# Performance work log

Measured on AMD Instinct MI355X. Metric: run time of the kernel, lower is better.

The kernel has to match this reference:

```python
import jax, jax.numpy as jnp
import numpy as np

B, S, D, H = 4, 2048, 1024, 16
HD = D // H

def setup_inputs() -> dict:
    key = jax.random.key(0)
    ks = jax.random.split(key, 12)
    std = 1.0 / np.sqrt(D)
    inp = {
        'query': jax.random.normal(ks[0], (B, S, D), jnp.float32),
        'key':   jax.random.normal(ks[1], (B, S, D), jnp.float32),
        'value': jax.random.normal(ks[2], (B, S, D), jnp.float32),
        'mask':  jnp.tril(jnp.ones((S, S), jnp.int32))[None, None, :, :],  # [1,1,S,S] causal
        'Wq': jax.random.uniform(ks[3], (D, D), jnp.float32, -std, std),
        'bq': jax.random.uniform(ks[4], (D,), jnp.float32, -std, std),
        'Wk': jax.random.uniform(ks[5], (D, D), jnp.float32, -std, std),
        'bk': jax.random.uniform(ks[6], (D,), jnp.float32, -std, std),
        'Wv': jax.random.uniform(ks[7], (D, D), jnp.float32, -std, std),
        'bv': jax.random.uniform(ks[8], (D,), jnp.float32, -std, std),
        'Wo': jax.random.uniform(ks[9], (D, D), jnp.float32, -std, std),
        'bo': jax.random.uniform(ks[10], (D,), jnp.float32, -std, std),
    }
    return inp

def _split_heads(x, W, b):
    # torch Linear: x @ W.T + b ; then [B,S,H,HD] -> [B,H,S,HD]
    y = jnp.einsum('bsd,ed->bse', x, W) + b
    return y.reshape(x.shape[0], -1, H, HD).transpose(0, 2, 1, 3)

def reference(query, key, value, mask, Wq, bq, Wk, bk, Wv, bv, Wo, bo):
    q = _split_heads(query, Wq, bq)   # [B,H,S,HD]
    k = _split_heads(key,   Wk, bk)
    v = _split_heads(value, Wv, bv)
    logits = jnp.einsum('bhqd,bhkd->bhqk', q, k) / np.sqrt(HD)  # [B,H,S,S]
    logits = jnp.where(mask == 0, jnp.float32(-1e9), logits)
    attn = jax.nn.softmax(logits, axis=-1)
    out = jnp.einsum('bhqk,bhkd->bhqd', attn, v)               # [B,H,S,HD]
    out = out.transpose(0, 2, 1, 3).reshape(query.shape[0], -1, D)
    return jnp.einsum('bsd,ed->bse', out, Wo) + bo
```

## Files before the change

### kernel.cpp

```cpp
#include <hip/hip_runtime.h>
#include <hip/hip_bf16.h>


#define SLEN 2048
#define DMOD 1024

typedef __attribute__((ext_vector_type(8))) short s16x8;
typedef __attribute__((ext_vector_type(4))) float f32x4;

__device__ __forceinline__ unsigned short f2bf(float f) {
    union { __hip_bfloat16 h; unsigned short u; } cv;
    cv.h = __float2bfloat16(f);
    return cv.u;
}
__device__ __forceinline__ unsigned cvtpk(float a, float b) {
    unsigned r;
    asm("v_cvt_pk_bf16_f32 %0, %1, %2" : "=v"(r) : "v"(a), "v"(b));
    return r;
}

__device__ __forceinline__ void gload_lds16(const void* g, void* l) {
    __builtin_amdgcn_global_load_lds(
        (const __attribute__((address_space(1))) void*)g,
        (__attribute__((address_space(3))) void*)l, 16, 0, 0);
}

__global__ __launch_bounds__(256) void convert_bf16(
    const float* __restrict__ q, const float* __restrict__ k,
    const float* __restrict__ v, const float* __restrict__ wq,
    const float* __restrict__ wk, const float* __restrict__ wv,
    const float* __restrict__ wo, unsigned short* __restrict__ ws)
{
    const int bid = blockIdx.x, tid = threadIdx.x;
    const float* src;
    unsigned short* dst;
    size_t off;
    if (bid < 3072) {
        const int t = bid >> 10;
        src = (t == 0) ? q : (t == 1) ? k : v;
        dst = ws + (size_t)t * 8388608;
        off = (size_t)(bid & 1023) * 8192;
    } else {
        const int w = (bid - 3072) >> 7;
        src = (w == 0) ? wq : (w == 1) ? wk : (w == 2) ? wv : wo;
        dst = ws + 25165824 + (size_t)w * 1048576;
        off = (size_t)((bid - 3072) & 127) * 8192;
    }
#pragma unroll
    for (int i = 0; i < 8; ++i) {
        const size_t e = off + (size_t)(i * 256 + tid) * 4;
        float4 x = *reinterpret_cast<const float4*>(&src[e]);
        uint2 u;
        u.x = cvtpk(x.x, x.y);
        u.y = cvtpk(x.z, x.w);
        *reinterpret_cast<uint2*>(&dst[e]) = u;
    }
}

template<int MODE>
__global__ __launch_bounds__(256) void gemm_bf16(
    const unsigned short* __restrict__ A, const unsigned short* __restrict__ W,
    const float* __restrict__ bias, void* __restrict__ outp, float oscale)
{
    __shared__ unsigned short Asm[2][8192];
    __shared__ unsigned short Bsm[2][8192];

    const int tid  = threadIdx.x;
    const int lane = tid & 63, wid = tid >> 6;
    const int l15 = lane & 15, lhi = lane >> 4;

    const int flat = blockIdx.x;
    const int logical = (flat & 7) * 64 + (flat >> 3);
    const int m0 = (logical >> 3) * 128, n0 = (logical & 7) * 128;

    const int wr = wid >> 1, wc = wid & 1;
    const int srow = lane >> 3;
    const int sgr  = (lane & 7) ^ srow;

    int aoff[2][4], boff[2][4];
#pragma unroll
    for (int kk = 0; kk < 2; ++kk)
#pragma unroll
        for (int i = 0; i < 4; ++i) {
            const int s = ((4 * kk + lhi) ^ (l15 & 7)) * 16;
            aoff[kk][i] = (wr * 64 + i * 16 + l15) * 128 + s;
            boff[kk][i] = (wc * 64 + i * 16 + l15) * 128 + s;
        }

    const unsigned short* apt = A + (size_t)(m0 + wid * 8 + srow) * 1024 + sgr * 8;
    const unsigned short* bpt = W + (size_t)(n0 + wid * 8 + srow) * 1024 + sgr * 8;

    f32x4 acc[4][4];
#pragma unroll
    for (int i = 0; i < 4; ++i)
#pragma unroll
        for (int j = 0; j < 4; ++j) acc[i][j] = (f32x4)0.f;

    auto stage = [&](int bsel) {
        char* ad = (char*)Asm + bsel * 16384 + wid * 1024;
        char* bd = (char*)Bsm + bsel * 16384 + wid * 1024;
#pragma unroll
        for (int i = 0; i < 4; ++i) {
            gload_lds16(apt + i * 32768, ad + i * 4096);
            gload_lds16(bpt + i * 32768, bd + i * 4096);
        }
        apt += 64; bpt += 64;
    };

    stage(0);
    __syncthreads();
    int cur = 0;
#pragma unroll 1
    for (int kt = 0; kt < 16; ++kt) {
        if (kt < 15) stage(cur ^ 1);
        const char* AB = (const char*)Asm + cur * 16384;
        const char* BB = (const char*)Bsm + cur * 16384;
#pragma unroll
        for (int kk = 0; kk < 2; ++kk) {
            s16x8 af[4], bfv[4];
#pragma unroll
            for (int i = 0; i < 4; ++i) af[i]  = *reinterpret_cast<const s16x8*>(AB + aoff[kk][i]);
#pragma unroll
            for (int j = 0; j < 4; ++j) bfv[j] = *reinterpret_cast<const s16x8*>(BB + boff[kk][j]);
#pragma unroll
            for (int i = 0; i < 4; ++i)
#pragma unroll
                for (int j = 0; j < 4; ++j)
                    acc[i][j] = __builtin_amdgcn_mfma_f32_16x16x32_bf16(af[i], bfv[j], acc[i][j], 0, 0, 0);
        }
        __syncthreads();
        cur ^= 1;
    }

#pragma unroll
    for (int j = 0; j < 4; ++j) {
        const int col = n0 + wc * 64 + j * 16 + l15;
        const float bv = bias[col];
#pragma unroll
        for (int i = 0; i < 4; ++i) {
#pragma unroll
            for (int r = 0; r < 4; ++r) {
                const int row = m0 + wr * 64 + i * 16 + lhi * 4 + r;
                const float val = (acc[i][j][r] + bv) * oscale;
                if constexpr (MODE == 2) {
                    ((float*)outp)[(size_t)row * 1024 + col] = val;
                } else if constexpr (MODE == 0) {
                    ((unsigned short*)outp)[(size_t)((row >> 11) * 16 + (col >> 6)) * 131072
                                            + (size_t)(row & 2047) * 64 + (col & 63)] = f2bf(val);
                } else {
                    ((unsigned short*)outp)[(size_t)((row >> 11) * 16 + (col >> 6)) * 131072
                                            + (size_t)(col & 63) * 2048 + (row & 2047)] = f2bf(val);
                }
            }
        }
    }
}

#define EXPC 0.18033688011112043f

__global__ __launch_bounds__(256, 4) void attn_kernel(
    const unsigned short* __restrict__ Q,
    const unsigned short* __restrict__ Kc,
    const unsigned short* __restrict__ Vt,
    unsigned short* __restrict__ Ao)
{
    __shared__ char smem[40960];

    const int tid = threadIdx.x, lane = tid & 63, wid = tid >> 6;
    const int l15 = lane & 15, lhi = lane >> 4;
    const int sK = l15 & 7;
    const int sub = lane >> 3, c8s = lane & 7;
    const int thr = wid * 16 + l15;

    const int kb0 = l15 * 128 + (lhi ^ sK) * 16;
    const int kb1 = kb0 ^ 64;
    char* const pb0 = smem + 32768 + wid * 2048 + kb0;
    char* const pb1 = smem + 32768 + wid * 2048 + kb1;
    char* const PWp = smem + 32768 + wid * 2048;
    int pw[4];
#pragma unroll
    for (int nb = 0; nb < 4; ++nb)
        pw[nb] = (l15 * 16 + ((nb * 4 + lhi) ^ (2 * sK))) * 8;

    const int flat = blockIdx.x;
    const int logical = (flat & 7) * 128 + (flat >> 3);
    const int bx = logical & 15, bh = logical >> 4;
    const int qtL = bx, qtH = 31 - bx;
    const int q0L = qtL * 64, q0H = qtH * 64;

    const size_t base = (size_t)bh * SLEN * 64;
    const unsigned short* Qb = Q + base;
    const unsigned short* Kb = Kc + base;
    const unsigned short* Vb = Vt + base;
    const int b = bh >> 4, h = bh & 15;
    const int scol = (c8s ^ sub) * 8;

    const f32x4 fzero = (f32x4)0.f;
    const s16x8 onesb = (s16x8)(short)0x3F80;

    s16x8 aqL[2], aqH[2];
#pragma unroll
    for (int kk = 0; kk < 2; ++kk) {
        aqL[kk] = *reinterpret_cast<const s16x8*>(
            &Qb[(size_t)(q0L + wid * 16 + l15) * 64 + kk * 32 + 8 * lhi]);
        aqH[kk] = *reinterpret_cast<const s16x8*>(
            &Qb[(size_t)(q0H + wid * 16 + l15) * 64 + kk * 32 + 8 * lhi]);
    }

    f32x4 oL[4], oH[4];
#pragma unroll
    for (int nb = 0; nb < 4; ++nb) { oL[nb] = (f32x4)0.f; oH[nb] = (f32x4)0.f; }
    f32x4 lL = (f32x4)0.f, lH = (f32x4)0.f;

    const unsigned short* kpt = Kb + (16 * wid + sub) * 64 + scol;
    const unsigned short* vpt = Vb + (size_t)(16 * wid + sub) * SLEN + scol;

    auto stage = [&](int bsel) {
        char* kd = smem + bsel * 8192 + wid * 2048;
        char* vd = smem + 16384 + bsel * 8192 + wid * 2048;
        gload_lds16(kpt,         kd);
        gload_lds16(kpt + 512,   kd + 1024);
        gload_lds16(vpt,         vd);
        gload_lds16(vpt + 16384, vd + 1024);
        kpt += 4096; vpt += 64;
    };

    auto tile = [&](s16x8 (&aq)[2], f32x4 (&o_acc)[4], f32x4& l_acc,
                    bool domask, const char* c0, const char* c1) {
        f32x4 sc2[4];
        __builtin_amdgcn_s_setprio(1);
        {
            s16x8 ak[4];
#pragma unroll
            for (int nb = 0; nb < 4; ++nb)
                ak[nb] = *reinterpret_cast<const s16x8*>(c0 + nb * 2048);
#pragma unroll
            for (int nb = 0; nb < 4; ++nb)
                sc2[nb] = __builtin_amdgcn_mfma_f32_16x16x32_bf16(ak[nb], aq[0], fzero, 0, 0, 0);
#pragma unroll
            for (int nb = 0; nb < 4; ++nb)
                ak[nb] = *reinterpret_cast<const s16x8*>(c1 + nb * 2048);
#pragma unroll
            for (int nb = 0; nb < 4; ++nb)
                sc2[nb] = __builtin_amdgcn_mfma_f32_16x16x32_bf16(ak[nb], aq[1], sc2[nb], 0, 0, 0);
        }
        __builtin_amdgcn_s_setprio(0);

        if (domask) {
#pragma unroll
            for (int nb = 0; nb < 4; ++nb)
#pragma unroll
                for (int r = 0; r < 4; ++r)
                    if (nb * 16 + lhi * 4 + r > thr) sc2[nb][r] = -1e30f;
        }

#pragma unroll
        for (int nb = 0; nb < 4; ++nb) {
            float p0 = exp2f(sc2[nb][0]);
            float p1 = exp2f(sc2[nb][1]);
            float p2 = exp2f(sc2[nb][2]);
            float p3 = exp2f(sc2[nb][3]);
            uint2 u;
            u.x = cvtpk(p0, p1);
            u.y = cvtpk(p2, p3);
            *reinterpret_cast<uint2*>(PWp + pw[nb]) = u;
        }

        __builtin_amdgcn_s_setprio(1);
#pragma unroll
        for (int kk = 0; kk < 2; ++kk) {
            s16x8 pa = *reinterpret_cast<const s16x8*>(kk ? pb1 : pb0);
            const char* vb = (kk ? c1 : c0) + 16384;
            s16x8 bvv[4];
#pragma unroll
            for (int nb = 0; nb < 4; ++nb)
                bvv[nb] = *reinterpret_cast<const s16x8*>(vb + nb * 2048);
#pragma unroll
            for (int nb = 0; nb < 4; ++nb)
                o_acc[nb] = __builtin_amdgcn_mfma_f32_16x16x32_bf16(pa, bvv[nb], o_acc[nb], 0, 0, 0);
            l_acc = __builtin_amdgcn_mfma_f32_16x16x32_bf16(pa, onesb, l_acc, 0, 0, 0);
        }
        __builtin_amdgcn_s_setprio(0);
    };

    stage(0);
    __syncthreads();
    int cur = 0;
    const int nt = qtH + 1;

#pragma unroll 1
    for (int t = 0; t < nt; ++t) {
        if (t + 1 < nt) stage(cur ^ 1);
        const char* c0 = smem + cur * 8192 + kb0;
        const char* c1 = smem + cur * 8192 + kb1;
        if (t <= qtL) tile(aqL, oL, lL, t == qtL, c0, c1);
        tile(aqH, oH, lH, t == qtH, c0, c1);
        __syncthreads();
        cur ^= 1;
    }

    float liL[4], liH[4];
#pragma unroll
    for (int r = 0; r < 4; ++r) { liL[r] = 1.0f / lL[r]; liH[r] = 1.0f / lH[r]; }
#pragma unroll
    for (int nb = 0; nb < 4; ++nb)
#pragma unroll
        for (int r = 0; r < 4; ++r) {
            const int sL = q0L + wid * 16 + lhi * 4 + r;
            const int sH = q0H + wid * 16 + lhi * 4 + r;
            const size_t cix = h * 64 + nb * 16 + l15;
            Ao[((size_t)b * SLEN + sL) * DMOD + cix] = f2bf(oL[nb][r] * liL[r]);
            Ao[((size_t)b * SLEN + sH) * DMOD + cix] = f2bf(oH[nb][r] * liH[r]);
        }
}

extern "C" void kernel_launch(void* const* d_in, const int* in_sizes, int n_in,
                              void* d_out, int out_size, void* d_ws, size_t ws_size,
                              hipStream_t stream) {
    const float* q  = (const float*)d_in[0];
    const float* k  = (const float*)d_in[1];
    const float* v  = (const float*)d_in[2];
    const float* Wq = (const float*)d_in[4];
    const float* bq = (const float*)d_in[5];
    const float* Wk = (const float*)d_in[6];
    const float* bk = (const float*)d_in[7];
    const float* Wv = (const float*)d_in[8];
    const float* bv = (const float*)d_in[9];
    const float* Wo = (const float*)d_in[10];
    const float* bo = (const float*)d_in[11];

    unsigned short* wsp = (unsigned short*)d_ws;
    unsigned short* qc  = wsp;
    unsigned short* kc  = wsp + 8388608;
    unsigned short* vc  = wsp + 16777216;
    unsigned short* wqc = wsp + 25165824;
    unsigned short* wkc = wsp + 26214400;
    unsigned short* wvc = wsp + 27262976;
    unsigned short* woc = wsp + 28311552;
    unsigned short* qb  = wsp + 29360128;
    unsigned short* kb  = wsp + 37748736;
    unsigned short* vtb = wsp + 46137344;
    unsigned short* ao  = qc;

    dim3 gb(256);
    convert_bf16<<<dim3(3584), gb, 0, stream>>>(q, k, v, Wq, Wk, Wv, Wo, wsp);
    gemm_bf16<0><<<dim3(512), gb, 0, stream>>>(qc, wqc, bq, qb, EXPC);
    gemm_bf16<0><<<dim3(512), gb, 0, stream>>>(kc, wkc, bk, kb, 1.0f);
    gemm_bf16<1><<<dim3(512), gb, 0, stream>>>(vc, wvc, bv, vtb, 1.0f);
    attn_kernel<<<dim3(1024), gb, 0, stream>>>(qb, kb, vtb, ao);
    gemm_bf16<2><<<dim3(512), gb, 0, stream>>>(ao, woc, bo, (float*)d_out, 1.0f);
}
```

Baseline: 178.8 us.

## Fuse fp32-to-bf16 activation conversion into QKV projection GEMM loads

```diff
diff --git a/kernel.cpp b/kernel.cpp
--- a/kernel.cpp
+++ b/kernel.cpp
@@ -25,27 +25,16 @@
         (__attribute__((address_space(3))) void*)l, 16, 0, 0);
 }
 
-__global__ __launch_bounds__(256) void convert_bf16(
-    const float* __restrict__ q, const float* __restrict__ k,
-    const float* __restrict__ v, const float* __restrict__ wq,
-    const float* __restrict__ wk, const float* __restrict__ wv,
-    const float* __restrict__ wo, unsigned short* __restrict__ ws)
+__global__ __launch_bounds__(256) void convert_w(
+    const float* __restrict__ wq, const float* __restrict__ wk,
+    const float* __restrict__ wv, const float* __restrict__ wo,
+    unsigned short* __restrict__ dst)
 {
     const int bid = blockIdx.x, tid = threadIdx.x;
-    const float* src;
-    unsigned short* dst;
-    size_t off;
-    if (bid < 3072) {
-        const int t = bid >> 10;
-        src = (t == 0) ? q : (t == 1) ? k : v;
-        dst = ws + (size_t)t * 8388608;
-        off = (size_t)(bid & 1023) * 8192;
-    } else {
-        const int w = (bid - 3072) >> 7;
-        src = (w == 0) ? wq : (w == 1) ? wk : (w == 2) ? wv : wo;
-        dst = ws + 25165824 + (size_t)w * 1048576;
-        off = (size_t)((bid - 3072) & 127) * 8192;
-    }
+    const int w = bid >> 7;
+    const float* src = (w == 0) ? wq : (w == 1) ? wk : (w == 2) ? wv : wo;
+    unsigned short* d = dst + (size_t)w * 1048576;
+    const size_t off = (size_t)(bid & 127) * 8192;
 #pragma unroll
     for (int i = 0; i < 8; ++i) {
         const size_t e = off + (size_t)(i * 256 + tid) * 4;
@@ -53,14 +42,140 @@
         uint2 u;
         u.x = cvtpk(x.x, x.y);
         u.y = cvtpk(x.z, x.w);
-        *reinterpret_cast<uint2*>(&dst[e]) = u;
+        *reinterpret_cast<uint2*>(&d[e]) = u;
     }
 }
 
 template<int MODE>
-__global__ __launch_bounds__(256) void gemm_bf16(
+__global__ __launch_bounds__(256) void gemm_qkv(
+    const float* __restrict__ A, const unsigned short* __restrict__ W,
+    const float* __restrict__ bias, unsigned short* __restrict__ outp,
+    float oscale)
+{
+    __shared__ unsigned short Asm[2][8192];
+    __shared__ unsigned short Bsm[2][8192];
+
+    const int tid  = threadIdx.x;
+    const int lane = tid & 63, wid = tid >> 6;
+    const int l15 = lane & 15, lhi = lane >> 4;
+
+    const int flat = blockIdx.x;
+    const int logical = (flat & 7) * 64 + (flat >> 3);
+    const int m0 = (logical >> 3) * 128, n0 = (logical & 7) * 128;
+    const int wr = wid >> 1, wc = wid & 1;
+
+    int soff[4];
+    const float* aptc[4];
+#pragma unroll
+    for (int i = 0; i < 4; ++i) {
+        const int f = i * 256 + tid;
+        const int srow = f >> 3, sg = f & 7;
+        soff[i] = srow * 128 + ((sg ^ (srow & 7)) * 16);
+        aptc[i] = A + (size_t)(m0 + srow) * 1024 + sg * 8;
+    }
+    const int wsrow = lane >> 3;
+    const int wsgr  = (lane & 7) ^ wsrow;
+    const unsigned short* bpt = W + (size_t)(n0 + wid * 8 + wsrow) * 1024 + wsgr * 8;
+
+    int aoff[2][4], boff[2][4];
+#pragma unroll
+    for (int kk = 0; kk < 2; ++kk)
+#pragma unroll
+        for (int i = 0; i < 4; ++i) {
+            const int s = ((4 * kk + lhi) ^ (l15 & 7)) * 16;
+            aoff[kk][i] = (wr * 64 + i * 16 + l15) * 128 + s;
+            boff[kk][i] = (wc * 64 + i * 16 + l15) * 128 + s;
+        }
+
+    f32x4 acc[4][4];
+#pragma unroll
+    for (int i = 0; i < 4; ++i)
+#pragma unroll
+        for (int j = 0; j < 4; ++j) acc[i][j] = (f32x4)0.f;
+
+    float4 aw[8];
+
+    auto loadA = [&](int k0) {
+#pragma unroll
+        for (int i = 0; i < 4; ++i) {
+            aw[2 * i]     = *reinterpret_cast<const float4*>(aptc[i] + k0);
+            aw[2 * i + 1] = *reinterpret_cast<const float4*>(aptc[i] + k0 + 4);
+        }
+    };
+    auto writeA = [&](int bsel) {
+#pragma unroll
+        for (int i = 0; i < 4; ++i) {
+            uint4 u;
+            u.x = cvtpk(aw[2 * i].x,     aw[2 * i].y);
+            u.y = cvtpk(aw[2 * i].z,     aw[2 * i].w);
+            u.z = cvtpk(aw[2 * i + 1].x, aw[2 * i + 1].y);
+            u.w = cvtpk(aw[2 * i + 1].z, aw[2 * i + 1].w);
+            *reinterpret_cast<uint4*>((char*)&Asm[bsel][0] + soff[i]) = u;
+        }
+    };
+    auto stageW = [&](int bsel) {
+        char* bd = (char*)Bsm + bsel * 16384 + wid * 1024;
+#pragma unroll
+        for (int i = 0; i < 4; ++i)
+            gload_lds16(bpt + i * 32768, bd + i * 4096);
+        bpt += 64;
+    };
+
+    loadA(0);
+    stageW(0);
+    writeA(0);
+    __syncthreads();
+
+#pragma unroll 1
+    for (int kt = 0; kt < 16; ++kt) {
+        if (kt < 15) {
+            loadA((kt + 1) * 64);
+            stageW((kt + 1) & 1);
+        }
+        const char* AB = (const char*)&Asm[kt & 1][0];
+        const char* BB = (const char*)&Bsm[kt & 1][0];
+#pragma unroll
+        for (int kk = 0; kk < 2; ++kk) {
+            s16x8 af[4], bfv[4];
+#pragma unroll
+            for (int i = 0; i < 4; ++i) af[i]  = *reinterpret_cast<const s16x8*>(AB + aoff[kk][i]);
+#pragma unroll
+            for (int j = 0; j < 4; ++j) bfv[j] = *reinterpret_cast<const s16x8*>(BB + boff[kk][j]);
+#pragma unroll
+            for (int i = 0; i < 4; ++i)
+#pragma unroll
+                for (int j = 0; j < 4; ++j)
+                    acc[i][j] = __builtin_amdgcn_mfma_f32_16x16x32_bf16(af[i], bfv[j], acc[i][j], 0, 0, 0);
+        }
+        if (kt < 15) writeA((kt + 1) & 1);
+        __syncthreads();
+    }
+
+#pragma unroll
+    for (int j = 0; j < 4; ++j) {
+        const int col = n0 + wc * 64 + j * 16 + l15;
+        const float bv = bias[col];
+#pragma unroll
+        for (int i = 0; i < 4; ++i) {
+#pragma unroll
+            for (int r = 0; r < 4; ++r) {
+                const int row = m0 + wr * 64 + i * 16 + lhi * 4 + r;
+                const float val = (acc[i][j][r] + bv) * oscale;
+                if constexpr (MODE == 0) {
+                    outp[(size_t)((row >> 11) * 16 + (col >> 6)) * 131072
+                         + (size_t)(row & 2047) * 64 + (col & 63)] = f2bf(val);
+                } else {
+                    outp[(size_t)((row >> 11) * 16 + (col >> 6)) * 131072
+                         + (size_t)(col & 63) * 2048 + (row & 2047)] = f2bf(val);
+                }
+            }
+        }
+    }
+}
+
+__global__ __launch_bounds__(256) void gemm_out(
     const unsigned short* __restrict__ A, const unsigned short* __restrict__ W,
-    const float* __restrict__ bias, void* __restrict__ outp, float oscale)
+    const float* __restrict__ bias, float* __restrict__ outp)
 {
     __shared__ unsigned short Asm[2][8192];
     __shared__ unsigned short Bsm[2][8192];
@@ -137,22 +252,12 @@
         const int col = n0 + wc * 64 + j * 16 + l15;
         const float bv = bias[col];
 #pragma unroll
-        for (int i = 0; i < 4; ++i) {
+        for (int i = 0; i < 4; ++i)
 #pragma unroll
             for (int r = 0; r < 4; ++r) {
                 const int row = m0 + wr * 64 + i * 16 + lhi * 4 + r;
-                const float val = (acc[i][j][r] + bv) * oscale;
-                if constexpr (MODE == 2) {
-                    ((float*)outp)[(size_t)row * 1024 + col] = val;
-                } else if constexpr (MODE == 0) {
-                    ((unsigned short*)outp)[(size_t)((row >> 11) * 16 + (col >> 6)) * 131072
-                                            + (size_t)(row & 2047) * 64 + (col & 63)] = f2bf(val);
-                } else {
-                    ((unsigned short*)outp)[(size_t)((row >> 11) * 16 + (col >> 6)) * 131072
-                                            + (size_t)(col & 63) * 2048 + (row & 2047)] = f2bf(val);
-                }
+                outp[(size_t)row * 1024 + col] = acc[i][j][r] + bv;
             }
-        }
     }
 }
 
@@ -330,23 +435,20 @@
     const float* bo = (const float*)d_in[11];
 
     unsigned short* wsp = (unsigned short*)d_ws;
-    unsigned short* qc  = wsp;
-    unsigned short* kc  = wsp + 8388608;
-    unsigned short* vc  = wsp + 16777216;
-    unsigned short* wqc = wsp + 25165824;
-    unsigned short* wkc = wsp + 26214400;
-    unsigned short* wvc = wsp + 27262976;
-    unsigned short* woc = wsp + 28311552;
-    unsigned short* qb  = wsp + 29360128;
-    unsigned short* kb  = wsp + 37748736;
-    unsigned short* vtb = wsp + 46137344;
-    unsigned short* ao  = qc;
+    unsigned short* wqc = wsp;
+    unsigned short* wkc = wsp + 1048576;
+    unsigned short* wvc = wsp + 2097152;
+    unsigned short* woc = wsp + 3145728;
+    unsigned short* qb  = wsp + 4194304;
+    unsigned short* kb  = wsp + 12582912;
+    unsigned short* vtb = wsp + 20971520;
+    unsigned short* ao  = wsp + 29360128;
 
     dim3 gb(256);
-    convert_bf16<<<dim3(3584), gb, 0, stream>>>(q, k, v, Wq, Wk, Wv, Wo, wsp);
-    gemm_bf16<0><<<dim3(512), gb, 0, stream>>>(qc, wqc, bq, qb, EXPC);
-    gemm_bf16<0><<<dim3(512), gb, 0, stream>>>(kc, wkc, bk, kb, 1.0f);
-    gemm_bf16<1><<<dim3(512), gb, 0, stream>>>(vc, wvc, bv, vtb, 1.0f);
+    convert_w<<<dim3(512), gb, 0, stream>>>(Wq, Wk, Wv, Wo, wsp);
+    gemm_qkv<0><<<dim3(512), gb, 0, stream>>>(q, wqc, bq, qb, EXPC);
+    gemm_qkv<0><<<dim3(512), gb, 0, stream>>>(k, wkc, bk, kb, 1.0f);
+    gemm_qkv<1><<<dim3(512), gb, 0, stream>>>(v, wvc, bv, vtb, 1.0f);
     attn_kernel<<<dim3(1024), gb, 0, stream>>>(qb, kb, vtb, ao);
-    gemm_bf16<2><<<dim3(512), gb, 0, stream>>>(ao, woc, bo, (float*)d_out, 1.0f);
-}
+    gemm_out<<<dim3(512), gb, 0, stream>>>(ao, woc, bo, (float*)d_out);
+}
```

Result: faster. 174.8 us (-2.3%).
